# Performance work log

Hardware: AMD Instinct MI355X
Metric: run time of the kernel (lower is better)

## Reference

```python
import jax, jax.numpy as jnp
import numpy as np

B, T, N, F = 16, 24, 2048, 64


def setup_inputs() -> dict:
    key = jax.random.key(0)
    kx, k1, k2, k3, kb, kv = jax.random.split(key, 6)
    x = jax.random.normal(kx, (B, T, N, F), dtype=jnp.float32)
    # xavier_uniform for U2 (N,F) and Ve (T,T); uniform(0,1) for U1, U3, be
    lim_u2 = float(np.sqrt(6.0 / (N + F)))
    lim_ve = float(np.sqrt(6.0 / (T + T)))
    U1 = jax.random.uniform(k1, (N,), dtype=jnp.float32)
    U2 = jax.random.uniform(k2, (N, F), dtype=jnp.float32, minval=-lim_u2, maxval=lim_u2)
    U3 = jax.random.uniform(k3, (F,), dtype=jnp.float32)
    be = jax.random.uniform(kb, (T, T), dtype=jnp.float32)
    Ve = jax.random.uniform(kv, (T, T), dtype=jnp.float32, minval=-lim_ve, maxval=lim_ve)
    return {"x": x, "U1": U1, "U2": U2, "U3": U3, "be": be, "Ve": Ve}


def reference(x, U1, U2, U3, be, Ve):
    # lhs: contract x over N with U1 -> (B,T,F), then project by U2^T -> (B,T,N)
    lhs = jnp.einsum('btnf,n->btf', x, U1) @ U2.T            # (B,T,N)
    # rhs: contract x over F with U3 -> (B,T,N)
    rhs = jnp.einsum('btnf,f->btn', x, U3)                   # (B,T,N)
    # temporal score matrix (B,T,T)
    product = jnp.einsum('btn,bsn->bts', lhs, rhs)
    E = jnp.einsum('ts,bsr->btr', Ve, jax.nn.sigmoid(product + be))
    A = jax.nn.softmax(E, axis=1)                            # softmax over dim=1 (t)
    # out[b,s,n,f] = sum_t x[b,t,n,f] * A[b,t,s]
    return jnp.einsum('btnf,bts->bsnf', x, A)
```

## Files before the change

kernel.cpp:

```cpp
#include <hip/hip_runtime.h>
#include <math.h>

#define BB 16
#define TT 24
#define NN 2048
#define FF 64
#define BT (BB*TT)
#define T2 (TT*TT)
#define NF4 (NN*FF/4)

#define WS_T1P  0
#define WS_R2P  (WS_T1P + 4*BT*FF)
#define WS_AMAT (WS_R2P + 4*BT*FF)

typedef float vfloat4 __attribute__((ext_vector_type(4)));

__device__ __forceinline__ float4 f4zero() { return make_float4(0.f,0.f,0.f,0.f); }

__device__ __forceinline__ void nt_store_f4(float4 v, float4* p) {
    vfloat4 nv;
    nv.x = v.x; nv.y = v.y; nv.z = v.z; nv.w = v.w;
    __builtin_nontemporal_store(nv, (vfloat4*)p);
}

__global__ __launch_bounds__(256) void k_stage1(
    const float4* __restrict__ x4, const float* __restrict__ U1,
    const float4* __restrict__ U3_4, const float4* __restrict__ U2_4,
    float4* __restrict__ t1p, float4* __restrict__ r2p)
{
    const int bt    = blockIdx.x;
    const int chunk = blockIdx.y;
    const int nbase = chunk * 512;
    const int tid   = threadIdx.x;
    const int wave  = tid >> 6;
    const int lane  = tid & 63;
    const int rowg  = lane >> 4;
    const int fq    = lane & 15;

    const float4 u3 = U3_4[fq];
    float4 t1a = f4zero();
    float4 r2a = f4zero();
    const float4* xb = x4 + (size_t)bt * NF4;

    for (int i = 0; i < 32; ++i) {
        const int n = nbase + i*16 + wave*4 + rowg;
        const float4 xv = xb[(size_t)n*16 + fq];
        const float u1n = U1[n];
        t1a.x += xv.x*u1n; t1a.y += xv.y*u1n; t1a.z += xv.z*u1n; t1a.w += xv.w*u1n;
        float r = xv.x*u3.x + xv.y*u3.y + xv.z*u3.z + xv.w*u3.w;
        r += __shfl_xor(r, 8);
        r += __shfl_xor(r, 4);
        r += __shfl_xor(r, 2);
        r += __shfl_xor(r, 1);
        const float4 u2 = U2_4[(size_t)n*16 + fq];
        r2a.x += r*u2.x; r2a.y += r*u2.y; r2a.z += r*u2.z; r2a.w += r*u2.w;
    }
    t1a.x += __shfl_xor(t1a.x, 16); t1a.y += __shfl_xor(t1a.y, 16);
    t1a.z += __shfl_xor(t1a.z, 16); t1a.w += __shfl_xor(t1a.w, 16);
    t1a.x += __shfl_xor(t1a.x, 32); t1a.y += __shfl_xor(t1a.y, 32);
    t1a.z += __shfl_xor(t1a.z, 32); t1a.w += __shfl_xor(t1a.w, 32);
    r2a.x += __shfl_xor(r2a.x, 16); r2a.y += __shfl_xor(r2a.y, 16);
    r2a.z += __shfl_xor(r2a.z, 16); r2a.w += __shfl_xor(r2a.w, 16);
    r2a.x += __shfl_xor(r2a.x, 32); r2a.y += __shfl_xor(r2a.y, 32);
    r2a.z += __shfl_xor(r2a.z, 32); r2a.w += __shfl_xor(r2a.w, 32);

    __shared__ float4 redT[4][16];
    __shared__ float4 redR[4][16];
    if (lane < 16) { redT[wave][lane] = t1a; redR[wave][lane] = r2a; }
    __syncthreads();
    if (tid < 16) {
        const float4 s0 = redT[0][tid], s1 = redT[1][tid], s2 = redT[2][tid], s3 = redT[3][tid];
        float4 tot;
        tot.x = s0.x+s1.x+s2.x+s3.x; tot.y = s0.y+s1.y+s2.y+s3.y;
        tot.z = s0.z+s1.z+s2.z+s3.z; tot.w = s0.w+s1.w+s2.w+s3.w;
        t1p[((size_t)chunk*BT + bt)*16 + tid] = tot;
    } else if (tid < 32) {
        const int q = tid - 16;
        const float4 s0 = redR[0][q], s1 = redR[1][q], s2 = redR[2][q], s3 = redR[3][q];
        float4 tot;
        tot.x = s0.x+s1.x+s2.x+s3.x; tot.y = s0.y+s1.y+s2.y+s3.y;
        tot.z = s0.z+s1.z+s2.z+s3.z; tot.w = s0.w+s1.w+s2.w+s3.w;
        r2p[((size_t)chunk*BT + bt)*16 + q] = tot;
    }
}

__global__ __launch_bounds__(576) void k_attn(
    const float* __restrict__ t1p, const float* __restrict__ r2p,
    const float* __restrict__ be, const float* __restrict__ Ve,
    float* __restrict__ Amat)
{
    const int b = blockIdx.x, tid = threadIdx.x;
    __shared__ float t1s[TT*FF];
    __shared__ float r2s[TT*65];
    __shared__ float VeL[T2];
    __shared__ float sigL[TT*25];
    __shared__ float EL[TT*25];
    __shared__ float eL[TT*25];

    for (int idx = tid; idx < TT*FF; idx += 576) {
        const size_t base = (size_t)b*TT*FF + idx;
        t1s[idx] = t1p[base] + t1p[base + BT*FF] + t1p[base + 2*BT*FF] + t1p[base + 3*BT*FF];
        const float s2 = r2p[base] + r2p[base + BT*FF] + r2p[base + 2*BT*FF] + r2p[base + 3*BT*FF];
        r2s[(idx >> 6)*65 + (idx & 63)] = s2;
    }
    VeL[tid] = Ve[tid];
    __syncthreads();

    const int i = tid / TT, j = tid % TT;
    float p = 0.f;
    #pragma unroll
    for (int f = 0; f < FF; ++f) p += t1s[i*FF + f] * r2s[j*65 + f];
    const float sg = 1.0f / (1.0f + expf(-(p + be[tid])));
    sigL[i*25 + j] = sg;
    __syncthreads();

    float E = 0.f;
    #pragma unroll
    for (int s = 0; s < TT; ++s) E += VeL[i*TT + s] * sigL[s*25 + j];
    EL[i*25 + j] = E;
    __syncthreads();

    float m = -1e30f;
    #pragma unroll
    for (int t = 0; t < TT; ++t) m = fmaxf(m, EL[t*25 + j]);
    const float e = expf(E - m);
    eL[i*25 + j] = e;
    __syncthreads();

    float ssum = 0.f;
    #pragma unroll
    for (int t = 0; t < TT; ++t) ssum += eL[t*25 + j];
    Amat[(size_t)b*T2 + tid] = e / ssum;
}

__global__ __launch_bounds__(256) void k_out(
    const float4* __restrict__ x4, const float4* __restrict__ Amat4,
    float4* __restrict__ out4)
{
    const int b   = blockIdx.y;
    const int idx = blockIdx.x*256 + threadIdx.x;

    __shared__ float4 A4[TT*6];
    if (threadIdx.x < TT*6) A4[threadIdx.x] = Amat4[(size_t)b*TT*6 + threadIdx.x];
    __syncthreads();

    const float4* xb = x4 + (size_t)b*TT*NF4;
    float4 acc[TT];
    #pragma unroll
    for (int s = 0; s < TT; ++s) acc[s] = f4zero();

    for (int t = 0; t < TT; ++t) {
        const float4 xv = xb[(size_t)t*NF4 + idx];
        #pragma unroll
        for (int sq = 0; sq < 6; ++sq) {
            const float4 a = A4[t*6 + sq];
            acc[4*sq+0].x += xv.x*a.x; acc[4*sq+0].y += xv.y*a.x;
            acc[4*sq+0].z += xv.z*a.x; acc[4*sq+0].w += xv.w*a.x;
            acc[4*sq+1].x += xv.x*a.y; acc[4*sq+1].y += xv.y*a.y;
            acc[4*sq+1].z += xv.z*a.y; acc[4*sq+1].w += xv.w*a.y;
            acc[4*sq+2].x += xv.x*a.z; acc[4*sq+2].y += xv.y*a.z;
            acc[4*sq+2].z += xv.z*a.z; acc[4*sq+2].w += xv.w*a.z;
            acc[4*sq+3].x += xv.x*a.w; acc[4*sq+3].y += xv.y*a.w;
            acc[4*sq+3].z += xv.z*a.w; acc[4*sq+3].w += xv.w*a.w;
        }
    }
    float4* ob = out4 + (size_t)b*TT*NF4;
    #pragma unroll
    for (int s = 0; s < TT; ++s)
        nt_store_f4(acc[s], &ob[(size_t)s*NF4 + idx]);
}

extern "C" void kernel_launch(void* const* d_in, const int* in_sizes, int n_in,
                              void* d_out, int out_size, void* d_ws, size_t ws_size,
                              hipStream_t stream)
{
    const float* x  = (const float*)d_in[0];
    const float* U1 = (const float*)d_in[1];
    const float* U2 = (const float*)d_in[2];
    const float* U3 = (const float*)d_in[3];
    const float* be = (const float*)d_in[4];
    const float* Ve = (const float*)d_in[5];

    float* ws   = (float*)d_ws;
    float* t1p  = ws + WS_T1P;
    float* r2p  = ws + WS_R2P;
    float* Am   = ws + WS_AMAT;

    k_stage1<<<dim3(BT, 4), 256, 0, stream>>>(
        (const float4*)x, U1, (const float4*)U3, (const float4*)U2,
        (float4*)t1p, (float4*)r2p);
    k_attn<<<dim3(BB), 576, 0, stream>>>(t1p, r2p, be, Ve, Am);
    k_out<<<dim3(NF4/256, BB), 256, 0, stream>>>(
        (const float4*)x, (const float4*)Am, (float4*)d_out);
}
```

Baseline: 380.1 us.

## Fuse attention-matrix computation into the output kernel, recomputed per block

Removes the separate single-wave-per-batch attention kernel and its workspace round trip. Each output block now rebuilds the 24x24 softmax attention matrix for its batch in shared memory before doing the weighted sum over time. This saves a kernel launch and a serial dependency stage. In exchange, every one of the many output blocks re-reads the stage-1 partial sums and repeats the score, sigmoid and softmax math, which adds L2 traffic and a per-block startup delay.

```diff
diff --git a/kernel.cpp b/kernel.cpp
--- a/kernel.cpp
+++ b/kernel.cpp
@@ -11,7 +11,6 @@
 
 #define WS_T1P  0
 #define WS_R2P  (WS_T1P + 4*BT*FF)
-#define WS_AMAT (WS_R2P + 4*BT*FF)
 
 typedef float vfloat4 __attribute__((ext_vector_type(4)));
 
@@ -84,67 +83,64 @@
     }
 }
 
-__global__ __launch_bounds__(576) void k_attn(
+__global__ __launch_bounds__(256) void k_out(
+    const float4* __restrict__ x4,
     const float* __restrict__ t1p, const float* __restrict__ r2p,
     const float* __restrict__ be, const float* __restrict__ Ve,
-    float* __restrict__ Amat)
+    float4* __restrict__ out4)
 {
-    const int b = blockIdx.x, tid = threadIdx.x;
+    const int b   = blockIdx.y;
+    const int tid = threadIdx.x;
+    const int idx = blockIdx.x*256 + tid;
+
     __shared__ float t1s[TT*FF];
     __shared__ float r2s[TT*65];
     __shared__ float VeL[T2];
     __shared__ float sigL[TT*25];
     __shared__ float EL[TT*25];
-    __shared__ float eL[TT*25];
+    __shared__ float Af[TT*TT];
 
-    for (int idx = tid; idx < TT*FF; idx += 576) {
-        const size_t base = (size_t)b*TT*FF + idx;
-        t1s[idx] = t1p[base] + t1p[base + BT*FF] + t1p[base + 2*BT*FF] + t1p[base + 3*BT*FF];
+    for (int q = tid; q < TT*FF; q += 256) {
+        const size_t base = (size_t)b*TT*FF + q;
+        t1s[q] = t1p[base] + t1p[base + BT*FF] + t1p[base + 2*BT*FF] + t1p[base + 3*BT*FF];
         const float s2 = r2p[base] + r2p[base + BT*FF] + r2p[base + 2*BT*FF] + r2p[base + 3*BT*FF];
-        r2s[(idx >> 6)*65 + (idx & 63)] = s2;
+        r2s[(q >> 6)*65 + (q & 63)] = s2;
     }
-    VeL[tid] = Ve[tid];
+    for (int q = tid; q < T2; q += 256) VeL[q] = Ve[q];
     __syncthreads();
 
-    const int i = tid / TT, j = tid % TT;
-    float p = 0.f;
-    #pragma unroll
-    for (int f = 0; f < FF; ++f) p += t1s[i*FF + f] * r2s[j*65 + f];
-    const float sg = 1.0f / (1.0f + expf(-(p + be[tid])));
-    sigL[i*25 + j] = sg;
+    for (int q = tid; q < T2; q += 256) {
+        const int i = q / TT, j = q % TT;
+        float p = 0.f;
+        #pragma unroll
+        for (int f = 0; f < FF; ++f) p += t1s[i*FF + f] * r2s[j*65 + f];
+        sigL[i*25 + j] = 1.0f / (1.0f + expf(-(p + be[q])));
+    }
     __syncthreads();
 
-    float E = 0.f;
-    #pragma unroll
-    for (int s = 0; s < TT; ++s) E += VeL[i*TT + s] * sigL[s*25 + j];
-    EL[i*25 + j] = E;
+    for (int q = tid; q < T2; q += 256) {
+        const int i = q / TT, j = q % TT;
+        float E = 0.f;
+        #pragma unroll
+        for (int s = 0; s < TT; ++s) E += VeL[i*TT + s] * sigL[s*25 + j];
+        EL[i*25 + j] = E;
+    }
     __syncthreads();
 
-    float m = -1e30f;
-    #pragma unroll
-    for (int t = 0; t < TT; ++t) m = fmaxf(m, EL[t*25 + j]);
-    const float e = expf(E - m);
-    eL[i*25 + j] = e;
-    __syncthreads();
-
-    float ssum = 0.f;
-    #pragma unroll
-    for (int t = 0; t < TT; ++t) ssum += eL[t*25 + j];
-    Amat[(size_t)b*T2 + tid] = e / ssum;
-}
-
-__global__ __launch_bounds__(256) void k_out(
-    const float4* __restrict__ x4, const float4* __restrict__ Amat4,
-    float4* __restrict__ out4)
-{
-    const int b   = blockIdx.y;
-    const int idx = blockIdx.x*256 + threadIdx.x;
-
-    __shared__ float4 A4[TT*6];
-    if (threadIdx.x < TT*6) A4[threadIdx.x] = Amat4[(size_t)b*TT*6 + threadIdx.x];
+    for (int q = tid; q < T2; q += 256) {
+        const int i = q / TT, j = q % TT;
+        float m = -1e30f;
+        #pragma unroll
+        for (int t = 0; t < TT; ++t) m = fmaxf(m, EL[t*25 + j]);
+        float ssum = 0.f;
+        #pragma unroll
+        for (int t = 0; t < TT; ++t) ssum += expf(EL[t*25 + j] - m);
+        Af[q] = expf(EL[i*25 + j] - m) / ssum;
+    }
     __syncthreads();
 
     const float4* xb = x4 + (size_t)b*TT*NF4;
+    const float4* A4 = (const float4*)Af;
     float4 acc[TT];
     #pragma unroll
     for (int s = 0; s < TT; ++s) acc[s] = f4zero();
@@ -184,12 +180,10 @@
     float* ws   = (float*)d_ws;
     float* t1p  = ws + WS_T1P;
     float* r2p  = ws + WS_R2P;
-    float* Am   = ws + WS_AMAT;
 
     k_stage1<<<dim3(BT, 4), 256, 0, stream>>>(
         (const float4*)x, U1, (const float4*)U3, (const float4*)U2,
         (float4*)t1p, (float4*)r2p);
-    k_attn<<<dim3(BB), 576, 0, stream>>>(t1p, r2p, be, Ve, Am);
     k_out<<<dim3(NF4/256, BB), 256, 0, stream>>>(
-        (const float4*)x, (const float4*)Am, (float4*)d_out);
+        (const float4*)x, t1p, r2p, be, Ve, (float4*)d_out);
 }
```

After: 387.7 us. Within noise of the previous version (+2.0%).
